# Kernel optimization log

Hardware: AMD Instinct MI355X
Metric: run time of the kernel (lower is better)

## Reference

```python
import jax, jax.numpy as jnp
from jax import lax
import numpy as np

PERCENTAGES = [0.004, 0.006, 0.008, 0.01, 0.012]
RADIUS = 1.0  # shape == 'square'
B, N = 4, 8192


def setup_inputs() -> dict:
    key = jax.random.key(0)
    adv_pcs = jax.random.uniform(key, (B, N, 3), dtype=jnp.float32)
    return {"adv_pcs": adv_pcs}


def _gather_points(pcs, idx):
    # pcs [B,N,3], idx [B,S] -> [B,S,3]
    idx3 = jnp.broadcast_to(idx[:, :, None], idx.shape + (3,))
    return jnp.take_along_axis(pcs, idx3, axis=1)


def farthest_point_sample(pcs, n_samples):
    # iterative FPS starting at index 0; returns indices [B, n_samples]
    Bb, Nn, _ = pcs.shape

    def step(carry, _):
        min_d2, last = carry  # [B,N], [B]
        p = _gather_points(pcs, last[:, None])  # [B,1,3]
        d2 = jnp.sum((pcs - p) ** 2, axis=-1)  # [B,N]
        min_d2 = jnp.minimum(min_d2, d2)
        nxt = jnp.argmax(min_d2, axis=-1).astype(jnp.int32)
        return (min_d2, nxt), last

    init = (jnp.full((Bb, Nn), 1e10, pcs.dtype), jnp.zeros((Bb,), jnp.int32))
    _, idx = lax.scan(step, init, None, length=n_samples)
    return jnp.transpose(idx)  # [B, n_samples]


def ball_query(seeds, pcs, r, K):
    # seeds [B,S,3], pcs [B,N,3] -> pts [B,S,K,3], idx [B,S,K] (-1 padded)
    d2 = jnp.sum((seeds[:, :, None, :] - pcs[:, None, :, :]) ** 2, axis=-1)  # [B,S,N]
    valid = d2 < r * r
    # stable sort: in-radius points first, preserving index order
    order = jnp.argsort(jnp.where(valid, 0, 1).astype(jnp.int32), axis=-1, stable=True)
    idx = order[..., :K]  # [B,S,K]
    cnt = jnp.sum(valid, axis=-1)  # [B,S]
    keep = jnp.arange(K)[None, None, :] < cnt[:, :, None]
    idx = jnp.where(keep, idx, -1)
    pts = jax.vmap(lambda p, i: p[i])(pcs, jnp.clip(idx, 0))  # [B,S,K,3]
    return pts, idx


def knn_second_sqdist(groups, lengths):
    # groups [G,K,3]; first `lengths[g]` rows of each group are valid candidates.
    # Returns squared distance to the 2nd nearest neighbor (incl. self at 0) [G,K].
    G, K, _ = groups.shape
    d2 = jnp.sum((groups[:, :, None, :] - groups[:, None, :, :]) ** 2, axis=-1)  # [G,K,K]
    col_ok = jnp.arange(K)[None, None, :] < lengths[:, None, None]
    d2 = jnp.where(col_ok, d2, jnp.inf)
    top2 = -lax.top_k(-d2, 2)[0]  # two smallest along candidates
    nn2 = top2[:, :, 1]  # second smallest (first is self, dist 0)
    return jnp.where(jnp.isfinite(nn2), nn2, 0.0)  # pad like pytorch3d (0 for missing)


def reference(adv_pcs):
    Bb, Nn, _ = adv_pcs.shape
    dt = adv_pcs.dtype
    seed_num = int(Nn * 0.05)
    fps_idx = farthest_point_sample(adv_pcs, seed_num)
    seeds = _gather_points(adv_pcs, fps_idx)  # [B,seed,3]
    loss = jnp.zeros((Bb,), dt)
    for p in PERCENTAGES:
        exp_num = Nn * p
        r = float(np.sqrt(p) * RADIUS)
        expect_dis = jnp.sqrt(jnp.asarray(np.pi * RADIUS ** 2 / exp_num * p, dt))
        K = int(2 * exp_num)
        pts, idx = ball_query(seeds, adv_pcs, r, K)
        pts = pts.reshape(Bb * seed_num, K, 3)
        idx = idx.reshape(Bb * seed_num, K)
        mask = idx != -1  # [G,K]
        gnum = jnp.sum(mask, axis=-1)  # [G], >= 1 (seed itself in-radius)
        nn2 = knn_second_sqdist(pts, gnum)  # [G,K] squared dists
        safe = jnp.where(nn2 > 0, nn2, 1.0)
        nn_dis = jnp.where(nn2 > 0, jnp.sqrt(safe), 0.0)
        clutter = jnp.square(nn_dis - expect_dis) / (expect_dis + 1e-12)
        # faithful to torch: sum over ALL elements, then elementwise divide by counts
        clutter_vec = jnp.sum(clutter * mask) / gnum.astype(dt)  # [G]
        imbalance = jnp.square(gnum.astype(dt) - exp_num) / exp_num  # [G]
        ul = (clutter_vec * imbalance).reshape(Bb, seed_num).mean(axis=-1)  # [B]
        loss = loss + ul
    return loss / len(PERCENTAGES)
```

## Files before the change

### kernel.cpp

```cpp
#include <hip/hip_runtime.h>
#include <math.h>

#define N_PTS 8192
#define B_SZ 4
#define SEED_NUM 409
#define FPS_THREADS 256
#define LTOT 653
#define N_GROUPS (B_SZ * SEED_NUM)

typedef float f2 __attribute__((ext_vector_type(2)));
typedef float f4 __attribute__((ext_vector_type(4)));

__device__ __forceinline__ float sqdist(float ax, float ay, float az,
                                        float bx, float by, float bz) {
  float dx = __fsub_rn(ax, bx);
  float dy = __fsub_rn(ay, by);
  float dz = __fsub_rn(az, bz);
  return __fadd_rn(__fadd_rn(__fmul_rn(dx, dx), __fmul_rn(dy, dy)),
                   __fmul_rn(dz, dz));
}

#define FOR16(M) \
  M(0) M(1) M(2) M(3) M(4) M(5) M(6) M(7) \
  M(8) M(9) M(10) M(11) M(12) M(13) M(14) M(15)

template <int CTRL>
__device__ __forceinline__ unsigned long long dpp_u64_bc1(
    unsigned long long k) {
  const unsigned lo2 = (unsigned)__builtin_amdgcn_update_dpp(
      0, (int)(unsigned)k, CTRL, 0xf, 0xf, true);
  const unsigned hi2 = (unsigned)__builtin_amdgcn_update_dpp(
      0, (int)(unsigned)(k >> 32), CTRL, 0xf, 0xf, true);
  return ((unsigned long long)hi2 << 32) | lo2;
}
template <int CTRL, int ROW_MASK>
__device__ __forceinline__ unsigned long long dpp_u64_keep(
    unsigned long long k) {
  const unsigned lo2 = (unsigned)__builtin_amdgcn_update_dpp(
      (int)(unsigned)k, (int)(unsigned)k, CTRL, ROW_MASK, 0xf, false);
  const unsigned hi2 = (unsigned)__builtin_amdgcn_update_dpp(
      (int)(unsigned)(k >> 32), (int)(unsigned)(k >> 32), CTRL, ROW_MASK, 0xf,
      false);
  return ((unsigned long long)hi2 << 32) | lo2;
}

__global__ __launch_bounds__(FPS_THREADS, 1) void fps_kernel(
    const float* __restrict__ pcs, float* __restrict__ seeds,
    double* __restrict__ sums ) {
#pragma clang fp contract(off)
  const int b = blockIdx.x;
  const int tid = threadIdx.x;
  const int lane = tid & 63, wid = tid >> 6;
  const float* base = pcs + (size_t)b * N_PTS * 3;

  if (b == 0 && tid < 26) sums[tid] = 0.0;

  __shared__ f4 spts4[N_PTS];
  __shared__ float seedbuf[SEED_NUM * 3];
  __shared__ unsigned long long red[2][4];

#define FPS_DECL(j) f2 px##j, py##j, pz##j, md##j;
  FOR16(FPS_DECL)
#undef FPS_DECL

#define FPS_INIT(j)                                   \
  {                                                   \
    const int i0 = tid + (2 * (j)) * FPS_THREADS;     \
    const int i1 = i0 + FPS_THREADS;                  \
    px##j = (f2){base[i0 * 3 + 0], base[i1 * 3 + 0]}; \
    py##j = (f2){base[i0 * 3 + 1], base[i1 * 3 + 1]}; \
    pz##j = (f2){base[i0 * 3 + 2], base[i1 * 3 + 2]}; \
    md##j = (f2){1e10f, 1e10f};   \
    spts4[i0] = (f4){px##j.x, py##j.x, pz##j.x, 0.f}; \
    spts4[i1] = (f4){px##j.y, py##j.y, pz##j.y, 0.f}; \
  }
  FOR16(FPS_INIT)
#undef FPS_INIT

#define FPS_PIN(j) asm volatile("" : "+v"(px##j), "+v"(py##j), "+v"(pz##j));
  FOR16(FPS_PIN)
#undef FPS_PIN

  float cx = base[0], cy = base[1], cz = base[2];

  for (int s = 0; s < SEED_NUM; ++s) {
    if (tid == 0) {
      seedbuf[s * 3 + 0] = cx;
      seedbuf[s * 3 + 1] = cy;
      seedbuf[s * 3 + 2] = cz;
    }
    const f2 ccx = (f2){cx, cx}, ccy = (f2){cy, cy}, ccz = (f2){cz, cz};
    float bv = -1.0f;
    int bi = 0;
#define FPS_UPD(j)                                                      \
  {                                                                     \
    const f2 dx = px##j - ccx;                                          \
    const f2 dy = py##j - ccy;                                          \
    const f2 dz = pz##j - ccz;                                          \
    const f2 t0 = dx * dx;                                              \
    const f2 t1 = dy * dy;                                              \
    const f2 t2 = dz * dz;                                              \
    const f2 d2 = (t0 + t1) + t2;                                       \
    const f2 m = __builtin_elementwise_min(md##j, d2);                  \
    md##j = m;                                                          \
    if (m.x > bv) { bv = m.x; bi = tid + (2 * (j)) * FPS_THREADS; }     \
    if (m.y > bv) { bv = m.y; bi = tid + (2 * (j) + 1) * FPS_THREADS; } \
  }
    FOR16(FPS_UPD)
#undef FPS_UPD
    unsigned long long key =
        ((unsigned long long)__float_as_uint(bv) << 32) |
        (unsigned long long)(unsigned)(N_PTS - 1 - bi);
    unsigned long long o;
    o = dpp_u64_bc1<0x111>(key);         key = (o > key) ? o : key;
    o = dpp_u64_bc1<0x112>(key);         key = (o > key) ? o : key;
    o = dpp_u64_bc1<0x114>(key);         key = (o > key) ? o : key;
    o = dpp_u64_bc1<0x118>(key);         key = (o > key) ? o : key;
    o = dpp_u64_keep<0x142, 0xa>(key);   key = (o > key) ? o : key;
    o = dpp_u64_keep<0x143, 0xc>(key);   key = (o > key) ? o : key;
    if (lane == 63) red[s & 1][wid] = key;
    __syncthreads();
    unsigned long long kmax = red[s & 1][0];
#pragma unroll
    for (int w = 1; w < 4; ++w) {
      const unsigned long long t = red[s & 1][w];
      kmax = (t > kmax) ? t : kmax;
    }
    const int ci = N_PTS - 1 - (int)(unsigned)(kmax & 0xffffffffull);
    const f4 c = spts4[ci];
    cx = c.x;
    cy = c.y;
    cz = c.z;
  }

  __syncthreads();
  float* sg = seeds + (size_t)b * SEED_NUM * 3;
  for (int i = tid; i < SEED_NUM * 3; i += FPS_THREADS) sg[i] = seedbuf[i];
}

__global__ __launch_bounds__(256) void group_kernel(
    const float* __restrict__ pcs, const float* __restrict__ seeds,
    double* __restrict__ totS , double* __restrict__ accA ,
    unsigned int* __restrict__ dcnt, float* __restrict__ out) {
  const int g = blockIdx.x;
  const int b = g / SEED_NUM;
  const int tid = threadIdx.x;
  const int lane = tid & 63, wid = tid >> 6;

  const int Kc[5] = {65, 98, 131, 163, 196};
  const int off[5] = {0, 65, 163, 294, 457};
  const double Pd[5] = {0.004, 0.006, 0.008, 0.01, 0.012};
  float r2c[5], expnf[5], expdc[5];
#pragma unroll
  for (int p = 0; p < 5; ++p) {
    const double pd = Pd[p];
    const double rd = sqrt(pd);
    r2c[p] = (float)(rd * rd);
    const double expn_d = 8192.0 * pd;
    expnf[p] = (float)expn_d;
    expdc[p] = sqrtf((float)(M_PI / expn_d * pd));
  }

  const float* base = pcs + (size_t)b * N_PTS * 3;
  const float* sp = seeds + (size_t)g * 3;
  const float sx = sp[0], sy = sp[1], sz = sp[2];

  __shared__ f4 tmp[LTOT];
  __shared__ f4 lpt[LTOT];
  __shared__ int tcnt[5], tbase[5], bcnt[5], ccum[5];
  __shared__ int ntmp, capped;
  __shared__ int wtot[4];
  __shared__ double wsum[5][4];
  __shared__ int islast;

  if (tid < 5) { tcnt[tid] = 0; bcnt[tid] = 0; }
  if (tid == 0) ntmp = 0;
  __syncthreads();

  const float r2max = r2c[4];
  const f4* base4 = (const f4*)base;
#define PROC(X, Y, Z)                                                       \
  {                                                                         \
    const float d2 = sqdist((X), (Y), (Z), sx, sy, sz);                     \
    if (d2 < r2max) {                                                       \
      const int tier = (d2 < r2c[0]) ? 0                                    \
                       : (d2 < r2c[1]) ? 1                                  \
                       : (d2 < r2c[2]) ? 2                                  \
                       : (d2 < r2c[3]) ? 3 : 4;                             \
      atomicAdd(&tcnt[tier], 1);                                            \
      const int pos = atomicAdd(&ntmp, 1);                                  \
      if (pos < LTOT) tmp[pos] = (f4){(X), (Y), (Z), (float)tier};          \
    }                                                                       \
  }
  for (int it = 0; it < 8; ++it) {
    const int q = it * 256 + tid;
    const f4 v0 = base4[q * 3 + 0];
    const f4 v1 = base4[q * 3 + 1];
    const f4 v2 = base4[q * 3 + 2];
    PROC(v0.x, v0.y, v0.z)
    PROC(v0.w, v1.x, v1.y)
    PROC(v1.z, v1.w, v2.x)
    PROC(v2.y, v2.z, v2.w)
  }
#undef PROC
  __syncthreads();

  if (tid == 0) {
    int acc = 0, cap = 0;
#pragma unroll
    for (int t = 0; t < 5; ++t) {
      tbase[t] = acc;
      acc += tcnt[t];
      ccum[t] = acc;
    }
#pragma unroll
    for (int p = 0; p < 5; ++p) cap |= (ccum[p] > Kc[p]) ? 1 : 0;
    capped = cap;
  }
  __syncthreads();

  const int nt = min(ntmp, LTOT);
  for (int t = tid; t < nt; t += 256) {
    const f4 e = tmp[t];
    const int tier = (int)e.w;
    const int pos = tbase[tier] + atomicAdd(&bcnt[tier], 1);
    if (pos < LTOT) lpt[pos] = (f4){e.x, e.y, e.z, 0.f};
  }
  __syncthreads();

  if (!capped) {
    const int c0 = ccum[0], c1 = ccum[1], c2 = ccum[2], c3 = ccum[3],
              c4 = ccum[4];
    double lS0 = 0.0, lS1 = 0.0, lS2 = 0.0, lS3 = 0.0, lS4 = 0.0;
    for (int r0 = 0; r0 < c4; r0 += 64) {
      const int row = r0 + (tid >> 2);
      const int sub = tid & 3;
      const bool rok = row < c4;
      const f4 pi = lpt[rok ? row : 0];
      float m1 = INFINITY, m2 = INFINITY;
      int j = sub;
#define SEGMENT(CP, EDP, LSP)                                               \
  {                                                                         \
    for (; j < (CP); j += 4) {                                              \
      const f4 pj = lpt[j];                                                 \
      const float d2 = sqdist(pi.x, pi.y, pi.z, pj.x, pj.y, pj.z);          \
      if (d2 < m1) { m2 = m1; m1 = d2; }                                    \
      else if (d2 < m2) { m2 = d2; }                                        \
    }                                                                       \
        \
    float s1 = m1, s2 = m2;                                                 \
    {                                                                       \
      const float o1 = __shfl_xor(s1, 1), o2 = __shfl_xor(s2, 1);           \
      const float lo = fminf(s1, o1), hi = fmaxf(s1, o1);                   \
      s2 = fminf(fminf(s2, o2), hi); s1 = lo;                               \
    }                                                                       \
    {                                                                       \
      const float o1 = __shfl_xor(s1, 2), o2 = __shfl_xor(s2, 2);           \
      const float lo = fminf(s1, o1), hi = fmaxf(s1, o1);                   \
      s2 = fminf(fminf(s2, o2), hi); s1 = lo;                               \
    }                                                                       \
    if (rok && sub == 0 && row < (CP)) {                                    \
      const float nn2 = (s2 > 1e37f) ? 0.0f : s2;             \
      const float nnd = (nn2 > 0.0f) ? sqrtf(nn2) : 0.0f;                   \
      const float diff = __fsub_rn(nnd, (EDP));                             \
      const float clut = __fdiv_rn(__fmul_rn(diff, diff),                   \
                                   __fadd_rn((EDP), 1e-12f));               \
      LSP += (double)clut;                                                  \
    }                                                                       \
  }
      SEGMENT(c0, expdc[0], lS0)
      SEGMENT(c1, expdc[1], lS1)
      SEGMENT(c2, expdc[2], lS2)
      SEGMENT(c3, expdc[3], lS3)
      SEGMENT(c4, expdc[4], lS4)
#undef SEGMENT
    }
#define RED(LSP, P)                                          \
  {                                                          \
    double v = (LSP);                                        \
    for (int o = 32; o > 0; o >>= 1) v += __shfl_down(v, o); \
    if (lane == 0) wsum[(P)][wid] = v;                       \
  }
    RED(lS0, 0) RED(lS1, 1) RED(lS2, 2) RED(lS3, 3) RED(lS4, 4)
#undef RED
  } else {
#pragma unroll
    for (int p = 0; p < 5; ++p) {
      int run = 0;
      for (int base_i = 0; base_i < N_PTS; base_i += 256) {
        const int i = base_i + tid;
        const float x = base[i * 3 + 0];
        const float y = base[i * 3 + 1];
        const float z = base[i * 3 + 2];
        const float d2 = sqdist(x, y, z, sx, sy, sz);
        const bool valid = d2 < r2c[p];
        const unsigned long long m = __ballot(valid);
        if (lane == 0) wtot[wid] = __popcll(m);
        __syncthreads();
        int pos = run + __popcll(m & ((1ull << lane) - 1ull));
        for (int w = 0; w < wid; ++w) pos += wtot[w];
        if (valid && pos < Kc[p]) {
          lpt[off[p] + pos] = (f4){x, y, z, 0.f};
        }
        run += wtot[0] + wtot[1] + wtot[2] + wtot[3];
        __syncthreads();
      }
    }
#pragma unroll
    for (int p = 0; p < 5; ++p) {
      const int gn = min(ccum[p], Kc[p]);
      const float ed = expdc[p];
      const int lb = off[p];
      double localS = 0.0;
      for (int r0 = 0; r0 < gn; r0 += 64) {
        const int row = r0 + (tid >> 2);
        const int sub = tid & 3;
        float m1 = INFINITY, m2 = INFINITY;
        if (row < gn) {
          const f4 pi = lpt[lb + row];
          for (int j = sub; j < gn; j += 4) {
            const f4 pj = lpt[lb + j];
            const float d2 = sqdist(pi.x, pi.y, pi.z, pj.x, pj.y, pj.z);
            if (d2 < m1) { m2 = m1; m1 = d2; }
            else if (d2 < m2) { m2 = d2; }
          }
        }
#pragma unroll
        for (int d = 1; d <= 2; d <<= 1) {
          const float om1 = __shfl_xor(m1, d);
          const float om2 = __shfl_xor(m2, d);
          const float lo = fminf(m1, om1);
          const float hi = fmaxf(m1, om1);
          m2 = fminf(fminf(m2, om2), hi);
          m1 = lo;
        }
        if (row < gn && sub == 0) {
          const float nn2 = (m2 > 1e37f) ? 0.0f : m2;
          const float nnd = (nn2 > 0.0f) ? sqrtf(nn2) : 0.0f;
          const float diff = __fsub_rn(nnd, ed);
          const float clut = __fdiv_rn(__fmul_rn(diff, diff),
                                       __fadd_rn(ed, 1e-12f));
          localS += (double)clut;
        }
      }
#pragma unroll
      for (int o = 32; o > 0; o >>= 1) localS += __shfl_down(localS, o);
      if (lane == 0) wsum[p][wid] = localS;
      __syncthreads();
    }
  }
  __syncthreads();

  if (tid < 5) {
    const double S = wsum[tid][0] + wsum[tid][1] + wsum[tid][2] + wsum[tid][3];
    atomicAdd(&totS[tid], S);
  } else if (tid < 10) {
    const int p = tid - 5;
    const int gn = min(ccum[p], Kc[p]);
    const float gf = (float)gn;
    const float dd = __fsub_rn(gf, expnf[p]);
    const float imb = __fdiv_rn(__fmul_rn(dd, dd), expnf[p]);
    atomicAdd(&accA[p * 4 + b], (double)imb / (double)gf);
  }

  __syncthreads();
  if (tid == 0) {
    __threadfence();
    const unsigned int old = atomicAdd(dcnt, 1u);
    islast = (old == (unsigned int)(N_GROUPS - 1)) ? 1 : 0;
  }
  __syncthreads();
  if (islast) {
    __shared__ double fin[25];
    if (tid < 25) {
      const double* src = (tid < 5) ? &totS[tid] : &accA[tid - 5];
      fin[tid] = atomicAdd((double*)src, 0.0);
    }
    __syncthreads();
    if (tid < B_SZ) {
      double acc = 0.0;
#pragma unroll
      for (int p = 0; p < 5; ++p)
        acc += fin[p] * (fin[5 + p * 4 + tid] / (double)SEED_NUM);
      out[tid] = (float)(acc / 5.0);
    }
  }
}

extern "C" void kernel_launch(void* const* d_in, const int* in_sizes, int n_in,
                              void* d_out, int out_size, void* d_ws,
                              size_t ws_size, hipStream_t stream) {
  (void)in_sizes; (void)n_in; (void)out_size; (void)ws_size;
  const float* pcs = (const float*)d_in[0];
  float* out = (float*)d_out;

  float* seeds = (float*)d_ws;
  double* sums = (double*)((char*)d_ws + 19632);

  fps_kernel<<<B_SZ, FPS_THREADS, 0, stream>>>(pcs, seeds, sums);
  group_kernel<<<N_GROUPS, 256, 0, stream>>>(
      pcs, seeds, sums, sums + 5, (unsigned int*)(sums + 25), out);
}
```

Before: 433.0 us.

## Fuse FPS and grouping into one persistent kernel with streamed seed publication

Merges the FPS kernel and the per-seed group kernel into a single launch. Block roles come from an atomic ticket: the first four blocks run FPS and publish seeds in chunks of 16 behind a release counter, and the remaining blocks spin-wait on that counter and then process their seed. This lets grouping overlap the serial FPS loop instead of waiting for it to finish. Shared memory is unioned across the two roles, and a memset resets the counters. The cost is spinning blocks occupying CUs, plus atomic seed writes and reads.

```diff
diff --git a/kernel.cpp b/kernel.cpp
--- a/kernel.cpp
+++ b/kernel.cpp
@@ -4,9 +4,10 @@
 #define N_PTS 8192
 #define B_SZ 4
 #define SEED_NUM 409
-#define FPS_THREADS 256
+#define THREADS 256
 #define LTOT 653
 #define N_GROUPS (B_SZ * SEED_NUM)
+#define PUB 16
 
 typedef float f2 __attribute__((ext_vector_type(2)));
 typedef float f4 __attribute__((ext_vector_type(4)));
@@ -44,29 +45,57 @@
   return ((unsigned long long)hi2 << 32) | lo2;
 }
 
-__global__ __launch_bounds__(FPS_THREADS, 1) void fps_kernel(
+struct FpsSmem {
+  f4 spts4[N_PTS];
+  float seedbuf[SEED_NUM * 3];
+  unsigned long long red[2][4];
+};
+struct GrpSmem {
+  f4 tmp[LTOT];
+  f4 lpt[LTOT];
+  int tcnt[5], tbase[5], bcnt[5], ccum[5];
+  int ntmp, capped;
+  int wtot[4];
+  double wsum[5][4];
+  float ssd[3];
+  int islast;
+};
+union SmemU {
+  FpsSmem f;
+  GrpSmem g;
+};
+
+__global__ __launch_bounds__(THREADS, 1) void fused_kernel(
     const float* __restrict__ pcs, float* __restrict__ seeds,
-    double* __restrict__ sums ) {
+    double* __restrict__ sums ,
+    unsigned int* __restrict__ ctr ,
+    float* __restrict__ out) {
 #pragma clang fp contract(off)
-  const int b = blockIdx.x;
   const int tid = threadIdx.x;
-  const int lane = tid & 63, wid = tid >> 6;
-  const float* base = pcs + (size_t)b * N_PTS * 3;
-
-  if (b == 0 && tid < 26) sums[tid] = 0.0;
-
-  __shared__ f4 spts4[N_PTS];
-  __shared__ float seedbuf[SEED_NUM * 3];
-  __shared__ unsigned long long red[2][4];
+  __shared__ SmemU sm;
+  __shared__ int roleS;
+  __shared__ double fin[25];
+
+  if (tid == 0) roleS = (int)atomicAdd(&ctr[0], 1u);
+  __syncthreads();
+  const int role = roleS;
+
+  if (role < B_SZ) {
+    const int b = role;
+    const int lane = tid & 63, wid = tid >> 6;
+    const float* base = pcs + (size_t)b * N_PTS * 3;
+    f4* spts4 = sm.f.spts4;
+    float* seedbuf = sm.f.seedbuf;
+    auto& red = sm.f.red;
 
 #define FPS_DECL(j) f2 px##j, py##j, pz##j, md##j;
-  FOR16(FPS_DECL)
+    FOR16(FPS_DECL)
 #undef FPS_DECL
 
 #define FPS_INIT(j)                                   \
   {                                                   \
-    const int i0 = tid + (2 * (j)) * FPS_THREADS;     \
-    const int i1 = i0 + FPS_THREADS;                  \
+    const int i0 = tid + (2 * (j)) * THREADS;         \
+    const int i1 = i0 + THREADS;                      \
     px##j = (f2){base[i0 * 3 + 0], base[i1 * 3 + 0]}; \
     py##j = (f2){base[i0 * 3 + 1], base[i1 * 3 + 1]}; \
     pz##j = (f2){base[i0 * 3 + 2], base[i1 * 3 + 2]}; \
@@ -74,77 +103,88 @@
     spts4[i0] = (f4){px##j.x, py##j.x, pz##j.x, 0.f}; \
     spts4[i1] = (f4){px##j.y, py##j.y, pz##j.y, 0.f}; \
   }
-  FOR16(FPS_INIT)
+    FOR16(FPS_INIT)
 #undef FPS_INIT
 
 #define FPS_PIN(j) asm volatile("" : "+v"(px##j), "+v"(py##j), "+v"(pz##j));
-  FOR16(FPS_PIN)
+    FOR16(FPS_PIN)
 #undef FPS_PIN
 
-  float cx = base[0], cy = base[1], cz = base[2];
-
-  for (int s = 0; s < SEED_NUM; ++s) {
+    float cx = base[0], cy = base[1], cz = base[2];
+
+    for (int s = 0; s < SEED_NUM; ++s) {
+      if (tid == 0) {
+        seedbuf[s * 3 + 0] = cx;
+        seedbuf[s * 3 + 1] = cy;
+        seedbuf[s * 3 + 2] = cz;
+        if ((s & (PUB - 1)) == (PUB - 1)) {
+          const int s0 = s - (PUB - 1);
+          float* sg = seeds + ((size_t)b * SEED_NUM + s0) * 3;
+          for (int i = 0; i < PUB * 3; ++i)
+            atomicExch(&sg[i], seedbuf[s0 * 3 + i]);
+          __hip_atomic_store(&ctr[2 + b], (unsigned)(s + 1),
+                             __ATOMIC_RELEASE, __HIP_MEMORY_SCOPE_AGENT);
+        }
+      }
+      const f2 ccx = (f2){cx, cx}, ccy = (f2){cy, cy}, ccz = (f2){cz, cz};
+      float bv = -1.0f;
+      int bi = 0;
+#define FPS_UPD(j)                                                  \
+  {                                                                 \
+    const f2 dx = px##j - ccx;                                      \
+    const f2 dy = py##j - ccy;                                      \
+    const f2 dz = pz##j - ccz;                                      \
+    const f2 t0 = dx * dx;                                          \
+    const f2 t1 = dy * dy;                                          \
+    const f2 t2 = dz * dz;                                          \
+    const f2 d2 = (t0 + t1) + t2;                                   \
+    const f2 m = __builtin_elementwise_min(md##j, d2);              \
+    md##j = m;                                                      \
+    if (m.x > bv) { bv = m.x; bi = tid + (2 * (j)) * THREADS; }     \
+    if (m.y > bv) { bv = m.y; bi = tid + (2 * (j) + 1) * THREADS; } \
+  }
+      FOR16(FPS_UPD)
+#undef FPS_UPD
+      unsigned long long key =
+          ((unsigned long long)__float_as_uint(bv) << 32) |
+          (unsigned long long)(unsigned)(N_PTS - 1 - bi);
+      unsigned long long o;
+      o = dpp_u64_bc1<0x111>(key);        key = (o > key) ? o : key;
+      o = dpp_u64_bc1<0x112>(key);        key = (o > key) ? o : key;
+      o = dpp_u64_bc1<0x114>(key);        key = (o > key) ? o : key;
+      o = dpp_u64_bc1<0x118>(key);        key = (o > key) ? o : key;
+      o = dpp_u64_keep<0x142, 0xa>(key);  key = (o > key) ? o : key;
+      o = dpp_u64_keep<0x143, 0xc>(key);  key = (o > key) ? o : key;
+      if (lane == 63) red[s & 1][wid] = key;
+      __syncthreads();
+      unsigned long long kmax = red[s & 1][0];
+#pragma unroll
+      for (int w = 1; w < 4; ++w) {
+        const unsigned long long t = red[s & 1][w];
+        kmax = (t > kmax) ? t : kmax;
+      }
+      const int ci = N_PTS - 1 - (int)(unsigned)(kmax & 0xffffffffull);
+      const f4 c = spts4[ci];
+      cx = c.x;
+      cy = c.y;
+      cz = c.z;
+    }
+
     if (tid == 0) {
-      seedbuf[s * 3 + 0] = cx;
-      seedbuf[s * 3 + 1] = cy;
-      seedbuf[s * 3 + 2] = cz;
-    }
-    const f2 ccx = (f2){cx, cx}, ccy = (f2){cy, cy}, ccz = (f2){cz, cz};
-    float bv = -1.0f;
-    int bi = 0;
-#define FPS_UPD(j)                                                      \
-  {                                                                     \
-    const f2 dx = px##j - ccx;                                          \
-    const f2 dy = py##j - ccy;                                          \
-    const f2 dz = pz##j - ccz;                                          \
-    const f2 t0 = dx * dx;                                              \
-    const f2 t1 = dy * dy;                                              \
-    const f2 t2 = dz * dz;                                              \
-    const f2 d2 = (t0 + t1) + t2;                                       \
-    const f2 m = __builtin_elementwise_min(md##j, d2);                  \
-    md##j = m;                                                          \
-    if (m.x > bv) { bv = m.x; bi = tid + (2 * (j)) * FPS_THREADS; }     \
-    if (m.y > bv) { bv = m.y; bi = tid + (2 * (j) + 1) * FPS_THREADS; } \
-  }
-    FOR16(FPS_UPD)
-#undef FPS_UPD
-    unsigned long long key =
-        ((unsigned long long)__float_as_uint(bv) << 32) |
-        (unsigned long long)(unsigned)(N_PTS - 1 - bi);
-    unsigned long long o;
-    o = dpp_u64_bc1<0x111>(key);         key = (o > key) ? o : key;
-    o = dpp_u64_bc1<0x112>(key);         key = (o > key) ? o : key;
-    o = dpp_u64_bc1<0x114>(key);         key = (o > key) ? o : key;
-    o = dpp_u64_bc1<0x118>(key);         key = (o > key) ? o : key;
-    o = dpp_u64_keep<0x142, 0xa>(key);   key = (o > key) ? o : key;
-    o = dpp_u64_keep<0x143, 0xc>(key);   key = (o > key) ? o : key;
-    if (lane == 63) red[s & 1][wid] = key;
-    __syncthreads();
-    unsigned long long kmax = red[s & 1][0];
-#pragma unroll
-    for (int w = 1; w < 4; ++w) {
-      const unsigned long long t = red[s & 1][w];
-      kmax = (t > kmax) ? t : kmax;
-    }
-    const int ci = N_PTS - 1 - (int)(unsigned)(kmax & 0xffffffffull);
-    const f4 c = spts4[ci];
-    cx = c.x;
-    cy = c.y;
-    cz = c.z;
-  }
-
-  __syncthreads();
-  float* sg = seeds + (size_t)b * SEED_NUM * 3;
-  for (int i = tid; i < SEED_NUM * 3; i += FPS_THREADS) sg[i] = seedbuf[i];
-}
-
-__global__ __launch_bounds__(256) void group_kernel(
-    const float* __restrict__ pcs, const float* __restrict__ seeds,
-    double* __restrict__ totS , double* __restrict__ accA ,
-    unsigned int* __restrict__ dcnt, float* __restrict__ out) {
-  const int g = blockIdx.x;
-  const int b = g / SEED_NUM;
-  const int tid = threadIdx.x;
+      const int s0 = SEED_NUM & ~(PUB - 1);
+      float* sg = seeds + ((size_t)b * SEED_NUM + s0) * 3;
+      for (int i = 0; i < (SEED_NUM - s0) * 3; ++i)
+        atomicExch(&sg[i], seedbuf[s0 * 3 + i]);
+      __hip_atomic_store(&ctr[2 + b], (unsigned)SEED_NUM, __ATOMIC_RELEASE,
+                         __HIP_MEMORY_SCOPE_AGENT);
+    }
+    return;
+  }
+
+  const int tk = role - B_SZ;
+  if (tk >= N_GROUPS) return;
+  const int s = tk >> 2;
+  const int b = tk & 3;
   const int lane = tid & 63, wid = tid >> 6;
 
   const int Kc[5] = {65, 98, 131, 163, 196};
@@ -162,35 +202,45 @@
   }
 
   const float* base = pcs + (size_t)b * N_PTS * 3;
-  const float* sp = seeds + (size_t)g * 3;
-  const float sx = sp[0], sy = sp[1], sz = sp[2];
-
-  __shared__ f4 tmp[LTOT];
-  __shared__ f4 lpt[LTOT];
-  __shared__ int tcnt[5], tbase[5], bcnt[5], ccum[5];
-  __shared__ int ntmp, capped;
-  __shared__ int wtot[4];
-  __shared__ double wsum[5][4];
-  __shared__ int islast;
+  f4* tmp = sm.g.tmp;
+  f4* lpt = sm.g.lpt;
+  int* tcnt = sm.g.tcnt;
+  int* tbase = sm.g.tbase;
+  int* bcnt = sm.g.bcnt;
+  int* ccum = sm.g.ccum;
+  int* wtot = sm.g.wtot;
+  double (*wsum)[4] = sm.g.wsum;
+  double* totS = sums;
+  double* accA = sums + 5;
 
   if (tid < 5) { tcnt[tid] = 0; bcnt[tid] = 0; }
-  if (tid == 0) ntmp = 0;
-  __syncthreads();
+  if (tid == 6) sm.g.ntmp = 0;
+  if (tid == 0) {
+    while (__hip_atomic_load(&ctr[2 + b], __ATOMIC_ACQUIRE,
+                             __HIP_MEMORY_SCOPE_AGENT) <= (unsigned)s)
+      __builtin_amdgcn_s_sleep(16);
+    const size_t so = ((size_t)b * SEED_NUM + s) * 3;
+    sm.g.ssd[0] = atomicAdd(&seeds[so + 0], 0.0f);
+    sm.g.ssd[1] = atomicAdd(&seeds[so + 1], 0.0f);
+    sm.g.ssd[2] = atomicAdd(&seeds[so + 2], 0.0f);
+  }
+  __syncthreads();
+  const float sx = sm.g.ssd[0], sy = sm.g.ssd[1], sz = sm.g.ssd[2];
 
   const float r2max = r2c[4];
   const f4* base4 = (const f4*)base;
-#define PROC(X, Y, Z)                                                       \
-  {                                                                         \
-    const float d2 = sqdist((X), (Y), (Z), sx, sy, sz);                     \
-    if (d2 < r2max) {                                                       \
-      const int tier = (d2 < r2c[0]) ? 0                                    \
-                       : (d2 < r2c[1]) ? 1                                  \
-                       : (d2 < r2c[2]) ? 2                                  \
-                       : (d2 < r2c[3]) ? 3 : 4;                             \
-      atomicAdd(&tcnt[tier], 1);                                            \
-      const int pos = atomicAdd(&ntmp, 1);                                  \
-      if (pos < LTOT) tmp[pos] = (f4){(X), (Y), (Z), (float)tier};          \
-    }                                                                       \
+#define PROC(X, Y, Z)                                              \
+  {                                                                \
+    const float d2 = sqdist((X), (Y), (Z), sx, sy, sz);            \
+    if (d2 < r2max) {                                              \
+      const int tier = (d2 < r2c[0]) ? 0                           \
+                       : (d2 < r2c[1]) ? 1                         \
+                       : (d2 < r2c[2]) ? 2                         \
+                       : (d2 < r2c[3]) ? 3 : 4;                    \
+      atomicAdd(&tcnt[tier], 1);                                   \
+      const int pos = atomicAdd(&sm.g.ntmp, 1);                    \
+      if (pos < LTOT) tmp[pos] = (f4){(X), (Y), (Z), (float)tier}; \
+    }                                                              \
   }
   for (int it = 0; it < 8; ++it) {
     const int q = it * 256 + tid;
@@ -215,11 +265,11 @@
     }
 #pragma unroll
     for (int p = 0; p < 5; ++p) cap |= (ccum[p] > Kc[p]) ? 1 : 0;
-    capped = cap;
-  }
-  __syncthreads();
-
-  const int nt = min(ntmp, LTOT);
+    sm.g.capped = cap;
+  }
+  __syncthreads();
+
+  const int nt = min(sm.g.ntmp, LTOT);
   for (int t = tid; t < nt; t += 256) {
     const f4 e = tmp[t];
     const int tier = (int)e.w;
@@ -228,7 +278,7 @@
   }
   __syncthreads();
 
-  if (!capped) {
+  if (!sm.g.capped) {
     const int c0 = ccum[0], c1 = ccum[1], c2 = ccum[2], c3 = ccum[3],
               c4 = ccum[4];
     double lS0 = 0.0, lS1 = 0.0, lS2 = 0.0, lS3 = 0.0, lS4 = 0.0;
@@ -239,34 +289,33 @@
       const f4 pi = lpt[rok ? row : 0];
       float m1 = INFINITY, m2 = INFINITY;
       int j = sub;
-#define SEGMENT(CP, EDP, LSP)                                               \
-  {                                                                         \
-    for (; j < (CP); j += 4) {                                              \
-      const f4 pj = lpt[j];                                                 \
-      const float d2 = sqdist(pi.x, pi.y, pi.z, pj.x, pj.y, pj.z);          \
-      if (d2 < m1) { m2 = m1; m1 = d2; }                                    \
-      else if (d2 < m2) { m2 = d2; }                                        \
-    }                                                                       \
-        \
-    float s1 = m1, s2 = m2;                                                 \
-    {                                                                       \
-      const float o1 = __shfl_xor(s1, 1), o2 = __shfl_xor(s2, 1);           \
-      const float lo = fminf(s1, o1), hi = fmaxf(s1, o1);                   \
-      s2 = fminf(fminf(s2, o2), hi); s1 = lo;                               \
-    }                                                                       \
-    {                                                                       \
-      const float o1 = __shfl_xor(s1, 2), o2 = __shfl_xor(s2, 2);           \
-      const float lo = fminf(s1, o1), hi = fmaxf(s1, o1);                   \
-      s2 = fminf(fminf(s2, o2), hi); s1 = lo;                               \
-    }                                                                       \
-    if (rok && sub == 0 && row < (CP)) {                                    \
-      const float nn2 = (s2 > 1e37f) ? 0.0f : s2;             \
-      const float nnd = (nn2 > 0.0f) ? sqrtf(nn2) : 0.0f;                   \
-      const float diff = __fsub_rn(nnd, (EDP));                             \
-      const float clut = __fdiv_rn(__fmul_rn(diff, diff),                   \
-                                   __fadd_rn((EDP), 1e-12f));               \
-      LSP += (double)clut;                                                  \
-    }                                                                       \
+#define SEGMENT(CP, EDP, LSP)                                        \
+  {                                                                  \
+    for (; j < (CP); j += 4) {                                       \
+      const f4 pj = lpt[j];                                          \
+      const float d2 = sqdist(pi.x, pi.y, pi.z, pj.x, pj.y, pj.z);   \
+      if (d2 < m1) { m2 = m1; m1 = d2; }                             \
+      else if (d2 < m2) { m2 = d2; }                                 \
+    }                                                                \
+    float s1 = m1, s2 = m2;                                          \
+    {                                                                \
+      const float o1 = __shfl_xor(s1, 1), o2 = __shfl_xor(s2, 1);    \
+      const float lo = fminf(s1, o1), hi = fmaxf(s1, o1);            \
+      s2 = fminf(fminf(s2, o2), hi); s1 = lo;                        \
+    }                                                                \
+    {                                                                \
+      const float o1 = __shfl_xor(s1, 2), o2 = __shfl_xor(s2, 2);    \
+      const float lo = fminf(s1, o1), hi = fmaxf(s1, o1);            \
+      s2 = fminf(fminf(s2, o2), hi); s1 = lo;                        \
+    }                                                                \
+    if (rok && sub == 0 && row < (CP)) {                             \
+      const float nn2 = (s2 > 1e37f) ? 0.0f : s2;      \
+      const float nnd = (nn2 > 0.0f) ? sqrtf(nn2) : 0.0f;            \
+      const float diff = __fsub_rn(nnd, (EDP));                      \
+      const float clut = __fdiv_rn(__fmul_rn(diff, diff),            \
+                                   __fadd_rn((EDP), 1e-12f));        \
+      LSP += (double)clut;                                           \
+    }                                                                \
   }
       SEGMENT(c0, expdc[0], lS0)
       SEGMENT(c1, expdc[1], lS1)
@@ -366,15 +415,14 @@
   __syncthreads();
   if (tid == 0) {
     __threadfence();
-    const unsigned int old = atomicAdd(dcnt, 1u);
-    islast = (old == (unsigned int)(N_GROUPS - 1)) ? 1 : 0;
-  }
-  __syncthreads();
-  if (islast) {
-    __shared__ double fin[25];
+    const unsigned int old = atomicAdd(&ctr[1], 1u);
+    sm.g.islast = (old == (unsigned int)(N_GROUPS - 1)) ? 1 : 0;
+  }
+  __syncthreads();
+  if (sm.g.islast) {
     if (tid < 25) {
-      const double* src = (tid < 5) ? &totS[tid] : &accA[tid - 5];
-      fin[tid] = atomicAdd((double*)src, 0.0);
+      double* src = (tid < 5) ? &totS[tid] : &accA[tid - 5];
+      fin[tid] = atomicAdd(src, 0.0);
     }
     __syncthreads();
     if (tid < B_SZ) {
@@ -396,8 +444,9 @@
 
   float* seeds = (float*)d_ws;
   double* sums = (double*)((char*)d_ws + 19632);
-
-  fps_kernel<<<B_SZ, FPS_THREADS, 0, stream>>>(pcs, seeds, sums);
-  group_kernel<<<N_GROUPS, 256, 0, stream>>>(
-      pcs, seeds, sums, sums + 5, (unsigned int*)(sums + 25), out);
+  unsigned int* ctr = (unsigned int*)((char*)d_ws + 19632 + 200);
+
+  hipMemsetAsync((char*)d_ws + 19632, 0, 200 + 24, stream);
+  fused_kernel<<<B_SZ + N_GROUPS, THREADS, 0, stream>>>(pcs, seeds, sums, ctr,
+                                                        out);
 }
```

After: 479.0 us. +10.6%, slower.
